# Kernel optimization log

Hardware: AMD Instinct MI355X
Metric: run time of the kernel (lower is better)

## Reference

```python
import jax, jax.numpy as jnp
import numpy as np
from jax.scipy.special import digamma, gammaln

COEF = 0.01
PRIOR = 1.0
IGNORE_INDEX = 255


def setup_inputs() -> dict:
    key = jax.random.key(0)
    k1, k2 = jax.random.split(key)
    pred = jax.random.normal(k1, (8, 19, 512, 512), dtype=jnp.float32)
    target = jax.random.randint(k2, (8, 512, 512), 0, 19, dtype=jnp.int64)
    return {"pred": pred, "target": target}


def reference(pred, target):
    # pred: [B, C, H, W] logits; target: [B, H, W] int class ids
    alphas = jnp.exp(pred)
    mask_ignore = target == IGNORE_INDEX
    tgt = jnp.where(mask_ignore, 0, target)
    # gather alpha at the answer class: [B, H, W]
    a_ans = jnp.take_along_axis(alphas, tgt[:, None, :, :], axis=1)[:, 0]
    a_zero = jnp.sum(alphas, axis=1)  # [B, H, W]
    ll_loss = digamma(a_ans) - digamma(a_zero)
    loss1 = gammaln(a_zero) - jnp.sum(gammaln(alphas), axis=1)
    loss2 = jnp.sum((alphas - PRIOR) * (digamma(alphas) - digamma(a_zero)[:, None, :, :]), axis=1)
    kl_loss = loss1 + loss2
    loss = COEF * kl_loss - ll_loss  # [B, H, W]
    loss = jnp.where(mask_ignore, jnp.zeros_like(loss), loss)
    avg_factor = jnp.sum(target != IGNORE_INDEX).astype(loss.dtype)
    return jnp.sum(loss) / avg_factor
```

## Files before the change

kernel.cpp:

```cpp
#include <hip/hip_runtime.h>


#define NCLS 19
#define HW (512 * 512)
#define NPIX (8 * HW)
#define NBLK 2048
#define IGNORE_IDX 255

#define PC1 0.08333333333f
#define PC2 0.00833333333f
#define PC3 0.00396825397f
#define GL1 0.08333333333f
#define GL2 0.00277777778f
#define GL3 0.00079365079f
#define HLN2PI 0.9189385332f
#define SUM_HLN2PI 17.45983213f

__device__ __forceinline__ float fast_rcp(float x) { return __builtin_amdgcn_rcpf(x); }

struct Acc {
    float a0, s2, slgx, dgans;
};

__device__ __forceinline__ void chan(float x, int c, int tc, Acc& A) {
    float a   = __expf(x);
    float y   = a + 1.f;
    float rpy = fast_rcp(a * y);
    float r   = a * rpy;
    float rp  = y * rpy;
    float ly  = __logf(y);
    float r2  = r * r;
    float T   = __fmaf_rn(-r2, __fmaf_rn(-r2, PC3, PC2), PC1);
    float psiy = __fmaf_rn(-r2, T, __fmaf_rn(-0.5f, r, ly));
    float psia = psiy - rp;
    A.s2 = __fmaf_rn(a - 1.f, psia, A.s2);
    A.a0 += a;
    float G   = __fmaf_rn(-r2, __fmaf_rn(-r2, GL3, GL2), GL1);
    float lgp = __fmaf_rn(y - 0.5f, ly, -y) - x;
    A.slgx = __fmaf_rn(r, G, A.slgx + lgp);
    A.dgans = (c == tc) ? psia : A.dgans;
}

__device__ __forceinline__ float finish(const Acc& A) {
    float a0  = A.a0;
    float y   = a0 + 1.f;
    float rpy = fast_rcp(a0 * y);
    float r   = a0 * rpy;
    float rp  = y * rpy;
    float ly  = __logf(y);
    float la  = __logf(a0);
    float r2  = r * r;
    float T   = __fmaf_rn(-r2, __fmaf_rn(-r2, PC3, PC2), PC1);
    float psi0 = __fmaf_rn(-r2, T, __fmaf_rn(-0.5f, r, ly)) - rp;
    float G   = __fmaf_rn(-r2, __fmaf_rn(-r2, GL3, GL2), GL1);
    float lg0 = __fmaf_rn(y - 0.5f, ly, -y) + HLN2PI + r * G - la;

    float sum_lg = A.slgx + SUM_HLN2PI;
    float ll    = A.dgans - psi0;
    float loss1 = lg0 - sum_lg;
    float loss2 = A.s2 - psi0 * (a0 - (float)NCLS);
    return 0.01f * (loss1 + loss2) - ll;
}

__global__ __launch_bounds__(256, 4) void bml_main(const float* __restrict__ pred,
                                                   const int* __restrict__ target,
                                                   float* __restrict__ partial) {
    int tid = blockIdx.x * blockDim.x + threadIdx.x;
    int p4  = tid << 2;
    int b   = p4 >> 18;
    int hw  = p4 & (HW - 1);
    const float4* base = (const float4*)(pred + (size_t)b * NCLS * HW + hw);

    float4 xs[NCLS];
    #pragma unroll
    for (int c = 0; c < NCLS; ++c)
        xs[c] = base[c * (HW / 4)];
    int4 t4 = *(const int4*)(target + p4);
    __builtin_amdgcn_sched_barrier(0);

    int tc0 = (t4.x == IGNORE_IDX) ? 0 : t4.x;
    int tc1 = (t4.y == IGNORE_IDX) ? 0 : t4.y;
    int tc2 = (t4.z == IGNORE_IDX) ? 0 : t4.z;
    int tc3 = (t4.w == IGNORE_IDX) ? 0 : t4.w;

    Acc A0 = {0.f, 0.f, 0.f, 0.f};
    Acc A1 = {0.f, 0.f, 0.f, 0.f};
    Acc A2 = {0.f, 0.f, 0.f, 0.f};
    Acc A3 = {0.f, 0.f, 0.f, 0.f};
    #pragma unroll
    for (int c = 0; c < NCLS; ++c) {
        chan(xs[c].x, c, tc0, A0);
        chan(xs[c].y, c, tc1, A1);
        chan(xs[c].z, c, tc2, A2);
        chan(xs[c].w, c, tc3, A3);
    }

    float l0 = finish(A0), l1 = finish(A1), l2 = finish(A2), l3 = finish(A3);

    float local = 0.f;
    float cnt = 0.f;
    if (t4.x != IGNORE_IDX) { local += l0; cnt += 1.f; }
    if (t4.y != IGNORE_IDX) { local += l1; cnt += 1.f; }
    if (t4.z != IGNORE_IDX) { local += l2; cnt += 1.f; }
    if (t4.w != IGNORE_IDX) { local += l3; cnt += 1.f; }

    #pragma unroll
    for (int off = 32; off; off >>= 1) {
        local += __shfl_down(local, off);
        cnt   += __shfl_down(cnt, off);
    }
    __shared__ float s_sum[4];
    __shared__ float s_cnt[4];
    int lane = threadIdx.x & 63, wid = threadIdx.x >> 6;
    if (lane == 0) { s_sum[wid] = local; s_cnt[wid] = cnt; }
    __syncthreads();
    if (threadIdx.x == 0) {
        partial[blockIdx.x]        = s_sum[0] + s_sum[1] + s_sum[2] + s_sum[3];
        partial[NBLK + blockIdx.x] = s_cnt[0] + s_cnt[1] + s_cnt[2] + s_cnt[3];
    }
}

__global__ __launch_bounds__(256) void bml_finalize(const float* __restrict__ partial,
                                                    float* __restrict__ out) {
    double s = 0.0, n = 0.0;
    for (int i = threadIdx.x; i < NBLK; i += 256) {
        s += (double)partial[i];
        n += (double)partial[NBLK + i];
    }
    #pragma unroll
    for (int off = 32; off; off >>= 1) {
        s += __shfl_down(s, off);
        n += __shfl_down(n, off);
    }
    __shared__ double sh_s[4], sh_n[4];
    int lane = threadIdx.x & 63, wid = threadIdx.x >> 6;
    if (lane == 0) { sh_s[wid] = s; sh_n[wid] = n; }
    __syncthreads();
    if (threadIdx.x == 0) {
        double ts = sh_s[0] + sh_s[1] + sh_s[2] + sh_s[3];
        double tn = sh_n[0] + sh_n[1] + sh_n[2] + sh_n[3];
        out[0] = (float)(ts / tn);
    }
}

extern "C" void kernel_launch(void* const* d_in, const int* in_sizes, int n_in,
                              void* d_out, int out_size, void* d_ws, size_t ws_size,
                              hipStream_t stream) {
    const float* pred = (const float*)d_in[0];
    const int* target = (const int*)d_in[1];
    float* out = (float*)d_out;
    float* partial = (float*)d_ws;

    const int block = 256;
    bml_main<<<NBLK, block, 0, stream>>>(pred, target, partial);
    bml_finalize<<<1, 256, 0, stream>>>(partial, out);
}
```

Measured before the change: 233.2 us.

## Stage channel loads through LDS via direct global-to-LDS DMA per step

Each block now processes 1024 pixels in four steps. Each wave issues global_load_lds DMA copies of its channels into a shared LDS tile, and every thread then computes one pixel from LDS instead of holding 19 float4 vectors in registers. This cuts register pressure so launch bounds can request 8 blocks per CU, aiming for higher occupancy and better latency hiding. In exchange, per-thread ILP drops from four pixels to one. Load and compute inside a block are serialized by barriers with no double buffering.

```diff
diff --git a/kernel.cpp b/kernel.cpp
--- a/kernel.cpp
+++ b/kernel.cpp
@@ -4,7 +4,9 @@
 #define NCLS 19
 #define HW (512 * 512)
 #define NPIX (8 * HW)
-#define NBLK 2048
+#define TPB 256
+#define STEPS 4
+#define NBLK (NPIX / (TPB * STEPS))
 #define IGNORE_IDX 255
 
 #define PC1 0.08333333333f
@@ -62,47 +64,42 @@
     return 0.01f * (loss1 + loss2) - ll;
 }
 
-__global__ __launch_bounds__(256, 4) void bml_main(const float* __restrict__ pred,
+__global__ __launch_bounds__(256, 8) void bml_main(const float* __restrict__ pred,
                                                    const int* __restrict__ target,
                                                    float* __restrict__ partial) {
-    int tid = blockIdx.x * blockDim.x + threadIdx.x;
-    int p4  = tid << 2;
-    int b   = p4 >> 18;
-    int hw  = p4 & (HW - 1);
-    const float4* base = (const float4*)(pred + (size_t)b * NCLS * HW + hw);
+    __shared__ float lds[NCLS * TPB];
 
-    float4 xs[NCLS];
-    #pragma unroll
-    for (int c = 0; c < NCLS; ++c)
-        xs[c] = base[c * (HW / 4)];
-    int4 t4 = *(const int4*)(target + p4);
-    __builtin_amdgcn_sched_barrier(0);
+    const int base_px = blockIdx.x * (TPB * STEPS);
+    const int b   = base_px >> 18;
+    const int hw0 = base_px & (HW - 1);
+    const float* pbase = pred + (size_t)b * NCLS * HW + hw0;
+    const int wave = threadIdx.x >> 6, lane = threadIdx.x & 63;
 
-    int tc0 = (t4.x == IGNORE_IDX) ? 0 : t4.x;
-    int tc1 = (t4.y == IGNORE_IDX) ? 0 : t4.y;
-    int tc2 = (t4.z == IGNORE_IDX) ? 0 : t4.z;
-    int tc3 = (t4.w == IGNORE_IDX) ? 0 : t4.w;
+    float local = 0.f, cnt = 0.f;
 
-    Acc A0 = {0.f, 0.f, 0.f, 0.f};
-    Acc A1 = {0.f, 0.f, 0.f, 0.f};
-    Acc A2 = {0.f, 0.f, 0.f, 0.f};
-    Acc A3 = {0.f, 0.f, 0.f, 0.f};
-    #pragma unroll
-    for (int c = 0; c < NCLS; ++c) {
-        chan(xs[c].x, c, tc0, A0);
-        chan(xs[c].y, c, tc1, A1);
-        chan(xs[c].z, c, tc2, A2);
-        chan(xs[c].w, c, tc3, A3);
+    for (int s = 0; s < STEPS; ++s) {
+        for (int c = wave; c < NCLS; c += 4) {
+            const float* g = pbase + (size_t)c * HW + s * TPB + lane * 4;
+            __builtin_amdgcn_global_load_lds(
+                (const __attribute__((address_space(1))) void*)g,
+                (__attribute__((address_space(3))) void*)&lds[c * TPB + lane * 4],
+                16, 0, 0);
+        }
+        int t = target[base_px + s * TPB + threadIdx.x];
+
+        __syncthreads();
+
+        int tc = (t == IGNORE_IDX) ? 0 : t;
+        Acc A = {0.f, 0.f, 0.f, 0.f};
+        #pragma unroll
+        for (int c = 0; c < NCLS; ++c)
+            chan(lds[c * TPB + threadIdx.x], c, tc, A);
+
+        float l = finish(A);
+        if (t != IGNORE_IDX) { local += l; cnt += 1.f; }
+
+        __syncthreads();
     }
-
-    float l0 = finish(A0), l1 = finish(A1), l2 = finish(A2), l3 = finish(A3);
-
-    float local = 0.f;
-    float cnt = 0.f;
-    if (t4.x != IGNORE_IDX) { local += l0; cnt += 1.f; }
-    if (t4.y != IGNORE_IDX) { local += l1; cnt += 1.f; }
-    if (t4.z != IGNORE_IDX) { local += l2; cnt += 1.f; }
-    if (t4.w != IGNORE_IDX) { local += l3; cnt += 1.f; }
 
     #pragma unroll
     for (int off = 32; off; off >>= 1) {
@@ -111,8 +108,7 @@
     }
     __shared__ float s_sum[4];
     __shared__ float s_cnt[4];
-    int lane = threadIdx.x & 63, wid = threadIdx.x >> 6;
-    if (lane == 0) { s_sum[wid] = local; s_cnt[wid] = cnt; }
+    if (lane == 0) { s_sum[wave] = local; s_cnt[wave] = cnt; }
     __syncthreads();
     if (threadIdx.x == 0) {
         partial[blockIdx.x]        = s_sum[0] + s_sum[1] + s_sum[2] + s_sum[3];
@@ -151,7 +147,6 @@
     float* out = (float*)d_out;
     float* partial = (float*)d_ws;
 
-    const int block = 256;
-    bml_main<<<NBLK, block, 0, stream>>>(pred, target, partial);
+    bml_main<<<NBLK, TPB, 0, stream>>>(pred, target, partial);
     bml_finalize<<<1, 256, 0, stream>>>(partial, out);
 }
```

Measured after the change: 237.2 us. No clear change (+1.7%).
